# Kernel tuning notes

Hardware: AMD Instinct MI355X
Metric: run time of the kernel (lower is better)

Reference implementation:

```python
import jax, jax.numpy as jnp
import numpy as np

VOCAB, EMBED, HIDDEN = 29, 64, 256
B, SEQ = 8, 257  # T = SEQ-1 = 256


def setup_inputs() -> dict:
    key = jax.random.key(0)
    ks = jax.random.split(key, 16)
    s = 0.02
    embed = jax.random.normal(ks[0], (VOCAB, EMBED), jnp.float32) * s
    embed = embed.at[0].set(0.0)  # padding_idx = PAD_TOKEN = 0
    d = dict(
        x=jax.random.randint(ks[1], (B, SEQ), 0, VOCAB),
        embed=embed,
        W_ih0=jax.random.normal(ks[2], (HIDDEN, EMBED), jnp.float32) * s,
        b_ih0=jax.random.normal(ks[3], (HIDDEN,), jnp.float32) * s,
        W_hh0=jax.random.normal(ks[4], (HIDDEN, HIDDEN), jnp.float32) * s,
        b_hh0=jax.random.normal(ks[5], (HIDDEN,), jnp.float32) * s,
        W_ih1=jax.random.normal(ks[6], (HIDDEN, HIDDEN), jnp.float32) * s,
        b_ih1=jax.random.normal(ks[7], (HIDDEN,), jnp.float32) * s,
        W_hh1=jax.random.normal(ks[8], (HIDDEN, HIDDEN), jnp.float32) * s,
        b_hh1=jax.random.normal(ks[9], (HIDDEN,), jnp.float32) * s,
        Wq=jax.random.normal(ks[10], (HIDDEN, HIDDEN), jnp.float32) * s,
        Wk=jax.random.normal(ks[11], (HIDDEN, HIDDEN), jnp.float32) * s,
        v=jax.random.normal(ks[12], (HIDDEN,), jnp.float32) * s,
        Wfc=jax.random.normal(ks[13], (VOCAB, 2 * HIDDEN), jnp.float32) * s,
        bfc=jax.random.normal(ks[14], (VOCAB,), jnp.float32) * s,
    )
    return d


def _forward(x, embed, W_ih0, b_ih0, W_hh0, b_hh0, W_ih1, b_ih1, W_hh1, b_hh1,
             Wq, Wk, v, Wfc, bfc):
    inp = x[:, :-1]                       # (B, T)
    emb = embed[inp]                      # (B, T, E); dropout = identity (eval)
    Bb, T, _ = emb.shape
    H = W_hh0.shape[0]

    # 2-layer Elman RNN via scan over time
    def step(carry, e_t):
        h0, h1 = carry
        h0 = jnp.tanh(e_t @ W_ih0.T + b_ih0 + h0 @ W_hh0.T + b_hh0)
        h1 = jnp.tanh(h0 @ W_ih1.T + b_ih1 + h1 @ W_hh1.T + b_hh1)
        return (h0, h1), h1

    init = (jnp.zeros((Bb, H), emb.dtype), jnp.zeros((Bb, H), emb.dtype))
    _, hs = jax.lax.scan(step, init, jnp.swapaxes(emb, 0, 1))  # (T, B, H)
    Hs = jnp.swapaxes(hs, 0, 1)           # (B, T, H) = all_hidden

    # Bahdanau additive self-attention over strictly-past hidden states
    q = Hs @ Wq.T                         # (B, T, H)
    k = Hs @ Wk.T                         # (B, T, H)
    e = jnp.tanh(q[:, :, None, :] + k[:, None, :, :])   # (B, T, T, H)
    scores = jnp.einsum('btsh,h->bts', e, v)             # (B, T, T)
    causal = jnp.tril(jnp.ones((T, T), bool), k=-1)      # s < t strictly
    scores = jnp.where(causal[None], scores, jnp.float32(-1e9))
    alpha = jax.nn.softmax(scores, axis=-1)
    ctx = jnp.einsum('bts,bsh->bth', alpha, Hs)          # (B, T, H)
    ctx = ctx * (jnp.arange(T) > 0)[None, :, None]       # t=0: zero context

    out = jnp.concatenate([Hs, ctx], axis=-1) @ Wfc.T + bfc  # (B, T, V)
    return out


def reference(x, embed, W_ih0, b_ih0, W_hh0, b_hh0, W_ih1, b_ih1, W_hh1, b_hh1,
              Wq, Wk, v, Wfc, bfc):
    return _forward(x, embed, W_ih0, b_ih0, W_hh0, b_hh0, W_ih1, b_ih1,
                    W_hh1, b_hh1, Wq, Wk, v, Wfc, bfc)
```

## Files before the change

kernel.cpp:

```cpp
#include <hip/hip_runtime.h>

#define HID   256
#define BATCH 8
#define TT    256
#define SEQL  257
#define VOCAB 29
#define EMB   64
#define TG    4
#define CH    8
#define NCHK  (TT / CH)

typedef _Float16 f16;
typedef f16  f16x8 __attribute__((ext_vector_type(8)));
typedef float f32x4 __attribute__((ext_vector_type(4)));

__device__ __forceinline__ float fast_tanh(float x) {
    float e = exp2f(x * 2.8853900817779268f);
    return 1.0f - 2.0f * __builtin_amdgcn_rcpf(1.0f + e);
}

__global__ __launch_bounds__(256) void pre0_kernel(
    const int* __restrict__ x, const float* __restrict__ embed,
    const float* __restrict__ Wih0, const float* __restrict__ bih0,
    const float* __restrict__ bhh0, float* __restrict__ C0, int* __restrict__ flags)
{
    if (blockIdx.x == 0 && threadIdx.x < 32) flags[threadIdx.x] = 0;
    int b  = blockIdx.x & 7;
    int t0 = (blockIdx.x >> 3) * 8;
    int tid = threadIdx.x;
    __shared__ float er[8][EMB];
    for (int idx = tid; idx < 8 * EMB; idx += 256) {
        int tt = idx >> 6, j = idx & 63;
        er[tt][j] = embed[x[b * SEQL + t0 + tt] * EMB + j];
    }
    __syncthreads();
    int i = tid;
    float base = bih0[i] + bhh0[i];
    float acc[8];
#pragma unroll
    for (int tt = 0; tt < 8; ++tt) acc[tt] = base;
    const float* wr = Wih0 + i * EMB;
    for (int j = 0; j < EMB; j += 4) {
        float4 w = *(const float4*)&wr[j];
#pragma unroll
        for (int tt = 0; tt < 8; ++tt) {
            float4 h = *(const float4*)&er[tt][j];
            acc[tt] += h.x * w.x + h.y * w.y + h.z * w.z + h.w * w.w;
        }
    }
#pragma unroll
    for (int tt = 0; tt < 8; ++tt)
        C0[((t0 + tt) * BATCH + b) * HID + i] = acc[tt];
}

__global__ __launch_bounds__(512) void mega_kernel(
    const float* __restrict__ Whh0, const float* __restrict__ Wih1,
    const float* __restrict__ Whh1, const float* __restrict__ bih1,
    const float* __restrict__ bhh1, const float* __restrict__ Wq,
    const float* __restrict__ Wk, const float* __restrict__ C0,
    float* __restrict__ Q, float* __restrict__ Hs,
    float* __restrict__ tkT, int* __restrict__ flags)
{
    __shared__ f16 hbuf[2][HID];
    __shared__ __align__(16) f16 stg[CH][HID];
    int tid = threadIdx.x;
    int wave = tid >> 6, lane = tid & 63;
    int lrow = lane & 15, lkg = lane >> 4;
    int role = blockIdx.x >> 3;
    int b = blockIdx.x & 7;
    int i0 = wave * 32 + lrow, i1 = i0 + 16;
    const f32x4 Z = {0.f, 0.f, 0.f, 0.f};

#define WAITF(idx, val)                                                             \
    {                                                                               \
        if (tid == 0) {                                                             \
            while (__hip_atomic_load(&flags[idx], __ATOMIC_ACQUIRE,                 \
                                     __HIP_MEMORY_SCOPE_AGENT) < (val))             \
                __builtin_amdgcn_s_sleep(2);                                        \
        }                                                                           \
        __syncthreads();                                                            \
    }
#define POSTF(idx, val)                                                             \
    {                                                                               \
        __syncthreads();                                                            \
        if (tid == 0) {                                                             \
            __hip_atomic_store(&flags[idx], (val), __ATOMIC_RELEASE,                \
                               __HIP_MEMORY_SCOPE_AGENT);                           \
        }                                                                           \
    }

    f16x8 a[8];
#pragma unroll
    for (int kt = 0; kt < 8; ++kt)
#pragma unroll
        for (int e = 0; e < 8; ++e) a[kt][e] = (f16)0.f;

    if (role == 0) {
        for (int idx = tid; idx < 2 * HID; idx += 512) ((f16*)hbuf)[idx] = (f16)0.f;
        f16x8 bf[8][2];
#pragma unroll
        for (int kt = 0; kt < 8; ++kt)
#pragma unroll
            for (int ct = 0; ct < 2; ++ct) {
                int n = wave * 32 + ct * 16 + lrow;
                const float* src = Whh0 + n * HID + kt * 32 + lkg * 8;
                f16x8 v;
#pragma unroll
                for (int e = 0; e < 8; ++e) v[e] = (f16)src[e];
                bf[kt][ct] = v;
            }
        __syncthreads();
        const float* cp = C0 + b * HID;
        float c0 = cp[i0], c1 = cp[i1];
        cp += BATCH * HID;
        f16* hp = (f16*)(Q + (size_t)b * TT * HID);

#define ASTEP(CUR, NXT)                                                             \
    {                                                                               \
        float cn0 = cp[i0];                                                         \
        float cn1 = cp[i1];                                                         \
        cp += BATCH * HID;                                                          \
        if (lrow == 0) {                                                            \
            _Pragma("unroll")                                                       \
            for (int kt = 0; kt < 8; ++kt)                                          \
                a[kt] = *(const f16x8*)&hbuf[CUR][kt * 32 + lkg * 8];               \
        }                                                                           \
        f32x4 p00 = __builtin_amdgcn_mfma_f32_16x16x32_f16(a[0], bf[0][0], Z, 0, 0, 0); \
        f32x4 p01 = __builtin_amdgcn_mfma_f32_16x16x32_f16(a[0], bf[0][1], Z, 0, 0, 0); \
        f32x4 p10 = __builtin_amdgcn_mfma_f32_16x16x32_f16(a[2], bf[2][0], Z, 0, 0, 0); \
        f32x4 p11 = __builtin_amdgcn_mfma_f32_16x16x32_f16(a[2], bf[2][1], Z, 0, 0, 0); \
        f32x4 p20 = __builtin_amdgcn_mfma_f32_16x16x32_f16(a[4], bf[4][0], Z, 0, 0, 0); \
        f32x4 p21 = __builtin_amdgcn_mfma_f32_16x16x32_f16(a[4], bf[4][1], Z, 0, 0, 0); \
        f32x4 p30 = __builtin_amdgcn_mfma_f32_16x16x32_f16(a[6], bf[6][0], Z, 0, 0, 0); \
        f32x4 p31 = __builtin_amdgcn_mfma_f32_16x16x32_f16(a[6], bf[6][1], Z, 0, 0, 0); \
        p00 = __builtin_amdgcn_mfma_f32_16x16x32_f16(a[1], bf[1][0], p00, 0, 0, 0); \
        p01 = __builtin_amdgcn_mfma_f32_16x16x32_f16(a[1], bf[1][1], p01, 0, 0, 0); \
        p10 = __builtin_amdgcn_mfma_f32_16x16x32_f16(a[3], bf[3][0], p10, 0, 0, 0); \
        p11 = __builtin_amdgcn_mfma_f32_16x16x32_f16(a[3], bf[3][1], p11, 0, 0, 0); \
        p20 = __builtin_amdgcn_mfma_f32_16x16x32_f16(a[5], bf[5][0], p20, 0, 0, 0); \
        p21 = __builtin_amdgcn_mfma_f32_16x16x32_f16(a[5], bf[5][1], p21, 0, 0, 0); \
        p30 = __builtin_amdgcn_mfma_f32_16x16x32_f16(a[7], bf[7][0], p30, 0, 0, 0); \
        p31 = __builtin_amdgcn_mfma_f32_16x16x32_f16(a[7], bf[7][1], p31, 0, 0, 0); \
        float v0 = fast_tanh(((p00[0] + p10[0]) + (p20[0] + p30[0])) + c0);         \
        float v1 = fast_tanh(((p01[0] + p11[0]) + (p21[0] + p31[0])) + c1);         \
        f16 hv0 = (f16)v0, hv1 = (f16)v1;                                           \
        if (lane < 16) {                                                            \
            hbuf[NXT][i0] = hv0;                                                    \
            hbuf[NXT][i1] = hv1;                                                    \
            hp[i0] = hv0;                                                           \
            hp[i1] = hv1;                                                           \
        }                                                                           \
        hp += 2 * HID;    \
        c0 = cn0; c1 = cn1;                                                         \
        asm volatile("s_waitcnt lgkmcnt(0)\n\ts_barrier" ::: "memory");             \
    }

        for (int ch = 0; ch < NCHK; ++ch) {
            ASTEP(0, 1) ASTEP(1, 0) ASTEP(0, 1) ASTEP(1, 0)
            ASTEP(0, 1) ASTEP(1, 0) ASTEP(0, 1) ASTEP(1, 0)
            if (ch & 1) POSTF(b, (ch + 1) >> 1)
        }
#undef ASTEP
    } else if (role == 1) {
        f16x8 bfI[8][2];
#pragma unroll
        for (int kt = 0; kt < 8; ++kt)
#pragma unroll
            for (int ct = 0; ct < 2; ++ct) {
                int n = wave * 32 + ct * 16 + lrow;
                const float* src = Wih1 + n * HID + kt * 32 + lkg * 8;
                f16x8 v;
#pragma unroll
                for (int e = 0; e < 8; ++e) v[e] = (f16)src[e];
                bfI[kt][ct] = v;
            }
        int col0 = wave * 32 + (lane & 15), col1 = col0 + 16;
        float bv0 = bih1[col0] + bhh1[col0];
        float bv1 = bih1[col1] + bhh1[col1];
        float* qb = Q + (size_t)b * TT * HID;

#define BBODY(CH_IDX)                                                               \
    {                                                                               \
        int ch = (CH_IDX);                                                          \
        if (tid < 256) {                                                            \
            int tp = tid >> 5, seg = tid & 31;                                      \
            *(f16x8*)&stg[tp][seg * 8] =                                            \
                *(const f16x8*)((const f16*)(qb + (size_t)(ch * CH + tp) * HID) + seg * 8); \
        }                                                                           \
        __syncthreads();                                                            \
        if (lrow < 8) {                                                             \
            _Pragma("unroll")                                                       \
            for (int kt = 0; kt < 8; ++kt)                                          \
                a[kt] = *(const f16x8*)&stg[lrow][kt * 32 + lkg * 8];               \
        }                                                                           \
        f32x4 u0 = __builtin_amdgcn_mfma_f32_16x16x32_f16(a[0], bfI[0][0], Z, 0, 0, 0); \
        f32x4 u1 = __builtin_amdgcn_mfma_f32_16x16x32_f16(a[0], bfI[0][1], Z, 0, 0, 0); \
        _Pragma("unroll")                                                           \
        for (int kt = 1; kt < 8; ++kt) {                                            \
            u0 = __builtin_amdgcn_mfma_f32_16x16x32_f16(a[kt], bfI[kt][0], u0, 0, 0, 0); \
            u1 = __builtin_amdgcn_mfma_f32_16x16x32_f16(a[kt], bfI[kt][1], u1, 0, 0, 0); \
        }                                                                           \
        if (lane < 32) {                                                            \
            float* co = qb + (size_t)(ch * CH + (lane >> 4) * 4) * HID;             \
            co[0 * HID + col0] = u0[0] + bv0;                                       \
            co[1 * HID + col0] = u0[1] + bv0;                                       \
            co[2 * HID + col0] = u0[2] + bv0;                                       \
            co[3 * HID + col0] = u0[3] + bv0;                                       \
            co[0 * HID + col1] = u1[0] + bv1;                                       \
            co[1 * HID + col1] = u1[1] + bv1;                                       \
            co[2 * HID + col1] = u1[2] + bv1;                                       \
            co[3 * HID + col1] = u1[3] + bv1;                                       \
        }                                                                           \
    }

        for (int chp = 0; chp < NCHK / 2; ++chp) {
            WAITF(b, chp + 1)
            BBODY(2 * chp)
            __syncthreads();
            BBODY(2 * chp + 1)
            POSTF(8 + b, chp + 1)
        }
#undef BBODY
    } else if (role == 2) {
        for (int idx = tid; idx < 2 * HID; idx += 512) ((f16*)hbuf)[idx] = (f16)0.f;
        f16x8 bf[8][2];
#pragma unroll
        for (int kt = 0; kt < 8; ++kt)
#pragma unroll
            for (int ct = 0; ct < 2; ++ct) {
                int n = wave * 32 + ct * 16 + lrow;
                const float* src = Whh1 + n * HID + kt * 32 + lkg * 8;
                f16x8 v;
#pragma unroll
                for (int e = 0; e < 8; ++e) v[e] = (f16)src[e];
                bf[kt][ct] = v;
            }
        __syncthreads();
        float* ho = Hs + (size_t)b * TT * HID;
        const float* cq = Q + (size_t)b * TT * HID;

#define CSTEP(CUR, NXT, CV0, CV1)                                                   \
    {                                                                               \
        if (lrow == 0) {                                                            \
            _Pragma("unroll")                                                       \
            for (int kt = 0; kt < 8; ++kt)                                          \
                a[kt] = *(const f16x8*)&hbuf[CUR][kt * 32 + lkg * 8];               \
        }                                                                           \
        f32x4 p00 = __builtin_amdgcn_mfma_f32_16x16x32_f16(a[0], bf[0][0], Z, 0, 0, 0); \
        f32x4 p01 = __builtin_amdgcn_mfma_f32_16x16x32_f16(a[0], bf[0][1], Z, 0, 0, 0); \
        f32x4 p10 = __builtin_amdgcn_mfma_f32_16x16x32_f16(a[2], bf[2][0], Z, 0, 0, 0); \
        f32x4 p11 = __builtin_amdgcn_mfma_f32_16x16x32_f16(a[2], bf[2][1], Z, 0, 0, 0); \
        f32x4 p20 = __builtin_amdgcn_mfma_f32_16x16x32_f16(a[4], bf[4][0], Z, 0, 0, 0); \
        f32x4 p21 = __builtin_amdgcn_mfma_f32_16x16x32_f16(a[4], bf[4][1], Z, 0, 0, 0); \
        f32x4 p30 = __builtin_amdgcn_mfma_f32_16x16x32_f16(a[6], bf[6][0], Z, 0, 0, 0); \
        f32x4 p31 = __builtin_amdgcn_mfma_f32_16x16x32_f16(a[6], bf[6][1], Z, 0, 0, 0); \
        p00 = __builtin_amdgcn_mfma_f32_16x16x32_f16(a[1], bf[1][0], p00, 0, 0, 0); \
        p01 = __builtin_amdgcn_mfma_f32_16x16x32_f16(a[1], bf[1][1], p01, 0, 0, 0); \
        p10 = __builtin_amdgcn_mfma_f32_16x16x32_f16(a[3], bf[3][0], p10, 0, 0, 0); \
        p11 = __builtin_amdgcn_mfma_f32_16x16x32_f16(a[3], bf[3][1], p11, 0, 0, 0); \
        p20 = __builtin_amdgcn_mfma_f32_16x16x32_f16(a[5], bf[5][0], p20, 0, 0, 0); \
        p21 = __builtin_amdgcn_mfma_f32_16x16x32_f16(a[5], bf[5][1], p21, 0, 0, 0); \
        p30 = __builtin_amdgcn_mfma_f32_16x16x32_f16(a[7], bf[7][0], p30, 0, 0, 0); \
        p31 = __builtin_amdgcn_mfma_f32_16x16x32_f16(a[7], bf[7][1], p31, 0, 0, 0); \
        float v0 = fast_tanh(((p00[0] + p10[0]) + (p20[0] + p30[0])) + CV0);        \
        float v1 = fast_tanh(((p01[0] + p11[0]) + (p21[0] + p31[0])) + CV1);        \
        if (lane < 16) {                                                            \
            hbuf[NXT][i0] = (f16)v0;                                                \
            hbuf[NXT][i1] = (f16)v1;                                                \
            ho[i0] = v0;                                                            \
            ho[i1] = v1;                                                            \
        }                                                                           \
        ho += HID;                                                                  \
        asm volatile("s_waitcnt lgkmcnt(0)\n\ts_barrier" ::: "memory");             \
    }

#define CCHUNK(CH_IDX)                                                              \
    {                                                                               \
        const float* cc = cq + (size_t)(CH_IDX) * CH * HID;                         \
        float d00 = cc[0*HID+i0], d01 = cc[0*HID+i1];                               \
        float d10 = cc[1*HID+i0], d11 = cc[1*HID+i1];                               \
        float d20 = cc[2*HID+i0], d21 = cc[2*HID+i1];                               \
        float d30 = cc[3*HID+i0], d31 = cc[3*HID+i1];                               \
        float d40 = cc[4*HID+i0], d41 = cc[4*HID+i1];                               \
        float d50 = cc[5*HID+i0], d51 = cc[5*HID+i1];                               \
        float d60 = cc[6*HID+i0], d61 = cc[6*HID+i1];                               \
        float d70 = cc[7*HID+i0], d71 = cc[7*HID+i1];                               \
        CSTEP(0, 1, d00, d01) CSTEP(1, 0, d10, d11)                                 \
        CSTEP(0, 1, d20, d21) CSTEP(1, 0, d30, d31)                                 \
        CSTEP(0, 1, d40, d41) CSTEP(1, 0, d50, d51)                                 \
        CSTEP(0, 1, d60, d61) CSTEP(1, 0, d70, d71)                                 \
    }

        for (int chp = 0; chp < NCHK / 2; ++chp) {
            WAITF(8 + b, chp + 1)
            CCHUNK(2 * chp)
            CCHUNK(2 * chp + 1)
            POSTF(16 + b, chp + 1)
        }
#undef CCHUNK
#undef CSTEP
    } else {
        const float* W = (role == 3) ? Wq : Wk;
        f16x8 bfW[8][2];
#pragma unroll
        for (int kt = 0; kt < 8; ++kt)
#pragma unroll
            for (int ct = 0; ct < 2; ++ct) {
                int n = wave * 32 + ct * 16 + lrow;
                const float* src = W + n * HID + kt * 32 + lkg * 8;
                f16x8 v;
#pragma unroll
                for (int e = 0; e < 8; ++e) v[e] = (f16)src[e];
                bfW[kt][ct] = v;
            }
        int col0 = wave * 32 + (lane & 15), col1 = col0 + 16;
        const float* hsb = Hs + (size_t)b * TT * HID;
        float* qb = Q + (size_t)b * TT * HID;

#define DEBODY(CH_IDX)                                                              \
    {                                                                               \
        int ch = (CH_IDX);                                                          \
        if (tid < 256) {                                                            \
            const float* src = hsb + (size_t)ch * CH * HID + tid * 8;               \
            float4 v0 = *(const float4*)&src[0];                                    \
            float4 v1 = *(const float4*)&src[4];                                    \
            f16x8 h = { (f16)v0.x, (f16)v0.y, (f16)v0.z, (f16)v0.w,                 \
                        (f16)v1.x, (f16)v1.y, (f16)v1.z, (f16)v1.w };               \
            *(f16x8*)((f16*)stg + tid * 8) = h;                                     \
        }                                                                           \
        __syncthreads();                                                            \
        if (lrow < 8) {                                                             \
            _Pragma("unroll")                                                       \
            for (int kt = 0; kt < 8; ++kt)                                          \
                a[kt] = *(const f16x8*)&stg[lrow][kt * 32 + lkg * 8];               \
        }                                                                           \
        f32x4 u0 = __builtin_amdgcn_mfma_f32_16x16x32_f16(a[0], bfW[0][0], Z, 0, 0, 0); \
        f32x4 u1 = __builtin_amdgcn_mfma_f32_16x16x32_f16(a[0], bfW[0][1], Z, 0, 0, 0); \
        _Pragma("unroll")                                                           \
        for (int kt = 1; kt < 8; ++kt) {                                            \
            u0 = __builtin_amdgcn_mfma_f32_16x16x32_f16(a[kt], bfW[kt][0], u0, 0, 0, 0); \
            u1 = __builtin_amdgcn_mfma_f32_16x16x32_f16(a[kt], bfW[kt][1], u1, 0, 0, 0); \
        }                                                                           \
        if (lane < 32) {                                                            \
            int tb2 = ch * CH + (lane >> 4) * 4;                                    \
            if (role == 3) {                                                        \
                float* co = qb + (size_t)tb2 * HID;                                 \
                co[0 * HID + col0] = fast_tanh(u0[0]);                              \
                co[1 * HID + col0] = fast_tanh(u0[1]);                              \
                co[2 * HID + col0] = fast_tanh(u0[2]);                              \
                co[3 * HID + col0] = fast_tanh(u0[3]);                              \
                co[0 * HID + col1] = fast_tanh(u1[0]);                              \
                co[1 * HID + col1] = fast_tanh(u1[1]);                              \
                co[2 * HID + col1] = fast_tanh(u1[2]);                              \
                co[3 * HID + col1] = fast_tanh(u1[3]);                              \
            } else {                                                                \
                float4 s0 = { fast_tanh(u0[0]), fast_tanh(u0[1]),                   \
                              fast_tanh(u0[2]), fast_tanh(u0[3]) };                 \
                float4 s1 = { fast_tanh(u1[0]), fast_tanh(u1[1]),                   \
                              fast_tanh(u1[2]), fast_tanh(u1[3]) };                 \
                *(float4*)&tkT[((size_t)b * HID + col0) * TT + tb2] = s0;           \
                *(float4*)&tkT[((size_t)b * HID + col1) * TT + tb2] = s1;           \
            }                                                                       \
        }                                                                           \
        __syncthreads();                                                            \
    }

        for (int chp = 0; chp < NCHK / 2; ++chp) {
            WAITF(16 + b, chp + 1)
            DEBODY(2 * chp + 0)
            DEBODY(2 * chp + 1)
        }
#undef DEBODY
    }
#undef WAITF
#undef POSTF
}

__global__ __launch_bounds__(256) void attn_kernel(
    const float* __restrict__ tq, const float* __restrict__ tkT,
    const float* __restrict__ vvec, const float* __restrict__ Hs,
    const float* __restrict__ Wfc, const float* __restrict__ bfc,
    float* __restrict__ out)
{
    int b  = blockIdx.x & 7;
    int t0 = (blockIdx.x >> 3) * TG;
    int tid = threadIdx.x;
    int wave = tid >> 6, lane = tid & 63;
    __shared__ float qs[TG][HID], vs[HID], alpha[TG][HID];
    __shared__ float cvec[TG][8][68];
    __shared__ float redm[4][TG], reds[4][TG];
#pragma unroll
    for (int j = 0; j < TG; ++j)
        qs[j][tid] = tq[((size_t)b * TT + t0 + j) * HID + tid];
    vs[tid] = vvec[tid];
    __syncthreads();

    float sc[TG];
#pragma unroll
    for (int j = 0; j < TG; ++j) sc[j] = -1e30f;
    if ((wave << 6) < t0 + TG) {
        const float* kT = tkT + (size_t)b * HID * TT + tid;
        float a0 = 0.f, a1 = 0.f, a2 = 0.f, a3 = 0.f;
        for (int jj = 0; jj < HID; jj += 4) {
            float k0 = kT[(size_t)(jj + 0) * TT];
            float k1 = kT[(size_t)(jj + 1) * TT];
            float k2 = kT[(size_t)(jj + 2) * TT];
            float k3 = kT[(size_t)(jj + 3) * TT];
            float4 vv = *(const float4*)&vs[jj];
            float4 q0 = *(const float4*)&qs[0][jj];
            float4 q1 = *(const float4*)&qs[1][jj];
            float4 q2 = *(const float4*)&qs[2][jj];
            float4 q3 = *(const float4*)&qs[3][jj];
#define TADD(qc, kc, vc, acc) { float num = qc + kc; float den = __builtin_fmaf(qc, kc, 1.f); acc += vc * num * __builtin_amdgcn_rcpf(den); }
            TADD(q0.x, k0, vv.x, a0) TADD(q0.y, k1, vv.y, a0) TADD(q0.z, k2, vv.z, a0) TADD(q0.w, k3, vv.w, a0)
            TADD(q1.x, k0, vv.x, a1) TADD(q1.y, k1, vv.y, a1) TADD(q1.z, k2, vv.z, a1) TADD(q1.w, k3, vv.w, a1)
            TADD(q2.x, k0, vv.x, a2) TADD(q2.y, k1, vv.y, a2) TADD(q2.z, k2, vv.z, a2) TADD(q2.w, k3, vv.w, a2)
            TADD(q3.x, k0, vv.x, a3) TADD(q3.y, k1, vv.y, a3) TADD(q3.z, k2, vv.z, a3) TADD(q3.w, k3, vv.w, a3)
#undef TADD
        }
        if (tid < t0 + 0) sc[0] = a0;
        if (tid < t0 + 1) sc[1] = a1;
        if (tid < t0 + 2) sc[2] = a2;
        if (tid < t0 + 3) sc[3] = a3;
    }
    float m0 = sc[0], m1 = sc[1], m2 = sc[2], m3 = sc[3];
#pragma unroll
    for (int off = 32; off; off >>= 1) {
        m0 = fmaxf(m0, __shfl_down(m0, off));
        m1 = fmaxf(m1, __shfl_down(m1, off));
        m2 = fmaxf(m2, __shfl_down(m2, off));
        m3 = fmaxf(m3, __shfl_down(m3, off));
    }
    if (lane == 0) { redm[wave][0] = m0; redm[wave][1] = m1; redm[wave][2] = m2; redm[wave][3] = m3; }
    __syncthreads();
    float ej[TG];
#pragma unroll
    for (int j = 0; j < TG; ++j) {
        float m = fmaxf(fmaxf(redm[0][j], redm[1][j]), fmaxf(redm[2][j], redm[3][j]));
        ej[j] = (tid < t0 + j) ? exp2f((sc[j] - m) * 1.4426950408889634f) : 0.f;
    }
    float z0 = ej[0], z1 = ej[1], z2 = ej[2], z3 = ej[3];
#pragma unroll
    for (int off = 32; off; off >>= 1) {
        z0 += __shfl_down(z0, off);
        z1 += __shfl_down(z1, off);
        z2 += __shfl_down(z2, off);
        z3 += __shfl_down(z3, off);
    }
    if (lane == 0) { reds[wave][0] = z0; reds[wave][1] = z1; reds[wave][2] = z2; reds[wave][3] = z3; }
    __syncthreads();
#pragma unroll
    for (int j = 0; j < TG; ++j) {
        float z = reds[0][j] + reds[1][j] + reds[2][j] + reds[3][j];
        alpha[j][tid] = (t0 + j == 0) ? 0.f : ej[j] * __builtin_amdgcn_rcpf(z);
    }
    __syncthreads();

    float c0 = 0.f, c1 = 0.f, c2 = 0.f, c3 = 0.f;
    const float* hb = Hs + (size_t)b * TT * HID;
    for (int s = 0; s < t0 + TG; s += 4) {
        float4 av0 = *(const float4*)&alpha[0][s];
        float4 av1 = *(const float4*)&alpha[1][s];
        float4 av2 = *(const float4*)&alpha[2][s];
        float4 av3 = *(const float4*)&alpha[3][s];
        float h0 = hb[(s + 0) * HID + tid];
        float h1 = hb[(s + 1) * HID + tid];
        float h2 = hb[(s + 2) * HID + tid];
        float h3 = hb[(s + 3) * HID + tid];
        c0 += av0.x * h0 + av0.y * h1 + av0.z * h2 + av0.w * h3;
        c1 += av1.x * h0 + av1.y * h1 + av1.z * h2 + av1.w * h3;
        c2 += av2.x * h0 + av2.y * h1 + av2.z * h2 + av2.w * h3;
        c3 += av3.x * h0 + av3.y * h1 + av3.z * h2 + av3.w * h3;
    }
    {
        int ph = tid >> 6, jj = tid & 63;
        cvec[0][ph][jj] = hb[(size_t)(t0 + 0) * HID + tid]; cvec[0][4 + ph][jj] = c0;
        cvec[1][ph][jj] = hb[(size_t)(t0 + 1) * HID + tid]; cvec[1][4 + ph][jj] = c1;
        cvec[2][ph][jj] = hb[(size_t)(t0 + 2) * HID + tid]; cvec[2][4 + ph][jj] = c2;
        cvec[3][ph][jj] = hb[(size_t)(t0 + 3) * HID + tid]; cvec[3][4 + ph][jj] = c3;
    }
    __syncthreads();

    if (tid < VOCAB * 8) {
        int o = tid >> 3, p = tid & 7;
        const float* wr = Wfc + o * 2 * HID + p * 64;
#pragma unroll
        for (int j = 0; j < TG; ++j) {
            const float* cv = &cvec[j][p][0];
            float a = 0.f;
            for (int jj = 0; jj < 64; jj += 4) {
                float4 w  = *(const float4*)&wr[jj];
                float4 cc = *(const float4*)&cv[jj];
                a += w.x * cc.x + w.y * cc.y + w.z * cc.z + w.w * cc.w;
            }
            a += __shfl_down(a, 4);
            a += __shfl_down(a, 2);
            a += __shfl_down(a, 1);
            if (p == 0) out[((size_t)b * TT + t0 + j) * VOCAB + o] = a + bfc[o];
        }
    }
}

extern "C" void kernel_launch(void* const* d_in, const int* in_sizes, int n_in,
                              void* d_out, int out_size, void* d_ws, size_t ws_size,
                              hipStream_t stream)
{
    (void)in_sizes; (void)n_in; (void)out_size; (void)ws_size;
    const int*   x     = (const int*)d_in[0];
    const float* embed = (const float*)d_in[1];
    const float* Wih0  = (const float*)d_in[2];
    const float* bih0  = (const float*)d_in[3];
    const float* Whh0  = (const float*)d_in[4];
    const float* bhh0  = (const float*)d_in[5];
    const float* Wih1  = (const float*)d_in[6];
    const float* bih1  = (const float*)d_in[7];
    const float* Whh1  = (const float*)d_in[8];
    const float* bhh1  = (const float*)d_in[9];
    const float* Wq    = (const float*)d_in[10];
    const float* Wk    = (const float*)d_in[11];
    const float* vvec  = (const float*)d_in[12];
    const float* Wfc   = (const float*)d_in[13];
    const float* bfc   = (const float*)d_in[14];
    float* out = (float*)d_out;
    float* ws  = (float*)d_ws;

    const size_t SZ = (size_t)TT * BATCH * HID;
    float* C0  = ws;
    float* Hs  = ws + SZ;
    float* Q   = ws + 2 * SZ;
    float* tkT = ws + 3 * SZ;
    int* flags = (int*)d_out;

    pre0_kernel<<<256, 256, 0, stream>>>(x, embed, Wih0, bih0, bhh0, C0, flags);
    mega_kernel<<<40, 512, 0, stream>>>(Whh0, Wih1, Whh1, bih1, bhh1, Wq, Wk,
                                        C0, Q, Hs, tkT, flags);
    attn_kernel<<<512, 256, 0, stream>>>(Q, tkT, vvec, Hs, Wfc, bfc, out);
}
```

Baseline: 209.7 us.

## Fuse attention into the persistent RNN kernel with flag-gated consumer blocks

Removes the separate attention kernel and appends its work as extra blocks of the mega kernel. Each attention block spin-waits on new per-batch Q/K progress flags that the projection roles now post. This lets attention for early timesteps overlap the remaining recurrence and removes a kernel launch boundary. Flags move from the output buffer to a device global, and shared memory becomes a union; the risks are that spinning blocks compete for CU resources with the producer blocks and that half of each 512-thread attention block sits idle.

```diff
diff --git a/kernel.cpp b/kernel.cpp
--- a/kernel.cpp
+++ b/kernel.cpp
@@ -14,6 +14,8 @@
 typedef f16  f16x8 __attribute__((ext_vector_type(8)));
 typedef float f32x4 __attribute__((ext_vector_type(4)));
 
+__device__ int g_flags[48];
+
 __device__ __forceinline__ float fast_tanh(float x) {
     float e = exp2f(x * 2.8853900817779268f);
     return 1.0f - 2.0f * __builtin_amdgcn_rcpf(1.0f + e);
@@ -22,9 +24,9 @@
 __global__ __launch_bounds__(256) void pre0_kernel(
     const int* __restrict__ x, const float* __restrict__ embed,
     const float* __restrict__ Wih0, const float* __restrict__ bih0,
-    const float* __restrict__ bhh0, float* __restrict__ C0, int* __restrict__ flags)
+    const float* __restrict__ bhh0, float* __restrict__ C0)
 {
-    if (blockIdx.x == 0 && threadIdx.x < 32) flags[threadIdx.x] = 0;
+    if (blockIdx.x == 0 && threadIdx.x < 48) g_flags[threadIdx.x] = 0;
     int b  = blockIdx.x & 7;
     int t0 = (blockIdx.x >> 3) * 8;
     int tid = threadIdx.x;
@@ -53,20 +55,25 @@
         C0[((t0 + tt) * BATCH + b) * HID + i] = acc[tt];
 }
 
+struct SmemM { f16 hbuf[2][HID]; __align__(16) f16 stg[CH][HID]; };
+struct SmemA { float qs[TG][HID]; float vs[HID]; float alpha[TG][HID];
+               float cvec[TG][8][68]; float redm[4][TG]; float reds[4][TG]; };
+union SmemU { SmemM m; SmemA a; };
+
 __global__ __launch_bounds__(512) void mega_kernel(
     const float* __restrict__ Whh0, const float* __restrict__ Wih1,
     const float* __restrict__ Whh1, const float* __restrict__ bih1,
     const float* __restrict__ bhh1, const float* __restrict__ Wq,
     const float* __restrict__ Wk, const float* __restrict__ C0,
-    float* __restrict__ Q, float* __restrict__ Hs,
-    float* __restrict__ tkT, int* __restrict__ flags)
+    float* __restrict__ Q, float* __restrict__ Hs, float* __restrict__ tkT,
+    const float* __restrict__ vvec, const float* __restrict__ Wfc,
+    const float* __restrict__ bfc, float* __restrict__ out)
 {
-    __shared__ f16 hbuf[2][HID];
-    __shared__ __align__(16) f16 stg[CH][HID];
+    __shared__ SmemU smem;
     int tid = threadIdx.x;
     int wave = tid >> 6, lane = tid & 63;
     int lrow = lane & 15, lkg = lane >> 4;
-    int role = blockIdx.x >> 3;
+    int role = (blockIdx.x < 40) ? (blockIdx.x >> 3) : 5;
     int b = blockIdx.x & 7;
     int i0 = wave * 32 + lrow, i1 = i0 + 16;
     const f32x4 Z = {0.f, 0.f, 0.f, 0.f};
@@ -74,7 +81,7 @@
 #define WAITF(idx, val)                                                             \
     {                                                                               \
         if (tid == 0) {                                                             \
-            while (__hip_atomic_load(&flags[idx], __ATOMIC_ACQUIRE,                 \
+            while (__hip_atomic_load(&g_flags[idx], __ATOMIC_ACQUIRE,               \
                                      __HIP_MEMORY_SCOPE_AGENT) < (val))             \
                 __builtin_amdgcn_s_sleep(2);                                        \
         }                                                                           \
@@ -84,7 +91,7 @@
     {                                                                               \
         __syncthreads();                                                            \
         if (tid == 0) {                                                             \
-            __hip_atomic_store(&flags[idx], (val), __ATOMIC_RELEASE,                \
+            __hip_atomic_store(&g_flags[idx], (val), __ATOMIC_RELEASE,              \
                                __HIP_MEMORY_SCOPE_AGENT);                           \
         }                                                                           \
     }
@@ -96,6 +103,7 @@
         for (int e = 0; e < 8; ++e) a[kt][e] = (f16)0.f;
 
     if (role == 0) {
+        f16 (*hbuf)[HID] = smem.m.hbuf;
         for (int idx = tid; idx < 2 * HID; idx += 512) ((f16*)hbuf)[idx] = (f16)0.f;
         f16x8 bf[8][2];
 #pragma unroll
@@ -162,6 +170,7 @@
         }
 #undef ASTEP
     } else if (role == 1) {
+        f16 (*stg)[HID] = smem.m.stg;
         f16x8 bfI[8][2];
 #pragma unroll
         for (int kt = 0; kt < 8; ++kt)
@@ -222,6 +231,7 @@
         }
 #undef BBODY
     } else if (role == 2) {
+        f16 (*hbuf)[HID] = smem.m.hbuf;
         for (int idx = tid; idx < 2 * HID; idx += 512) ((f16*)hbuf)[idx] = (f16)0.f;
         f16x8 bf[8][2];
 #pragma unroll
@@ -299,7 +309,8 @@
         }
 #undef CCHUNK
 #undef CSTEP
-    } else {
+    } else if (role <= 4) {
+        f16 (*stg)[HID] = smem.m.stg;
         const float* W = (role == 3) ? Wq : Wk;
         f16x8 bfW[8][2];
 #pragma unroll
@@ -369,136 +380,146 @@
             WAITF(16 + b, chp + 1)
             DEBODY(2 * chp + 0)
             DEBODY(2 * chp + 1)
+            POSTF(24 + (role - 3) * 8 + b, chp + 1)
         }
 #undef DEBODY
+    } else {
+        int aidx = blockIdx.x - 40;
+        int ab = aidx & 7;
+        int t0 = (aidx >> 3) * TG;
+        int p_need = (t0 + TG + 15) / 16;
+        WAITF(24 + ab, p_need)
+        WAITF(32 + ab, p_need)
+
+        float (*qs)[HID]     = smem.a.qs;
+        float* vs            = smem.a.vs;
+        float (*alpha)[HID]  = smem.a.alpha;
+        float (*cvec)[8][68] = smem.a.cvec;
+        float (*redm)[TG]    = smem.a.redm;
+        float (*reds)[TG]    = smem.a.reds;
+        const float* tq = Q;
+
+        if (tid < HID) {
+#pragma unroll
+            for (int j = 0; j < TG; ++j)
+                qs[j][tid] = tq[((size_t)ab * TT + t0 + j) * HID + tid];
+            vs[tid] = vvec[tid];
+        }
+        __syncthreads();
+
+        float sc[TG];
+#pragma unroll
+        for (int j = 0; j < TG; ++j) sc[j] = -1e30f;
+        if ((wave << 6) < t0 + TG) {
+            const float* kT = tkT + (size_t)ab * HID * TT + tid;
+            float a0 = 0.f, a1 = 0.f, a2 = 0.f, a3 = 0.f;
+            for (int jj = 0; jj < HID; jj += 4) {
+                float k0 = kT[(size_t)(jj + 0) * TT];
+                float k1 = kT[(size_t)(jj + 1) * TT];
+                float k2 = kT[(size_t)(jj + 2) * TT];
+                float k3 = kT[(size_t)(jj + 3) * TT];
+                float4 vv = *(const float4*)&vs[jj];
+                float4 q0 = *(const float4*)&qs[0][jj];
+                float4 q1 = *(const float4*)&qs[1][jj];
+                float4 q2 = *(const float4*)&qs[2][jj];
+                float4 q3 = *(const float4*)&qs[3][jj];
+#define TADD(qc, kc, vc, acc) { float num = qc + kc; float den = __builtin_fmaf(qc, kc, 1.f); acc += vc * num * __builtin_amdgcn_rcpf(den); }
+                TADD(q0.x, k0, vv.x, a0) TADD(q0.y, k1, vv.y, a0) TADD(q0.z, k2, vv.z, a0) TADD(q0.w, k3, vv.w, a0)
+                TADD(q1.x, k0, vv.x, a1) TADD(q1.y, k1, vv.y, a1) TADD(q1.z, k2, vv.z, a1) TADD(q1.w, k3, vv.w, a1)
+                TADD(q2.x, k0, vv.x, a2) TADD(q2.y, k1, vv.y, a2) TADD(q2.z, k2, vv.z, a2) TADD(q2.w, k3, vv.w, a2)
+                TADD(q3.x, k0, vv.x, a3) TADD(q3.y, k1, vv.y, a3) TADD(q3.z, k2, vv.z, a3) TADD(q3.w, k3, vv.w, a3)
+#undef TADD
+            }
+            if (tid < t0 + 0) sc[0] = a0;
+            if (tid < t0 + 1) sc[1] = a1;
+            if (tid < t0 + 2) sc[2] = a2;
+            if (tid < t0 + 3) sc[3] = a3;
+        }
+        float m0 = sc[0], m1 = sc[1], m2 = sc[2], m3 = sc[3];
+#pragma unroll
+        for (int off = 32; off; off >>= 1) {
+            m0 = fmaxf(m0, __shfl_down(m0, off));
+            m1 = fmaxf(m1, __shfl_down(m1, off));
+            m2 = fmaxf(m2, __shfl_down(m2, off));
+            m3 = fmaxf(m3, __shfl_down(m3, off));
+        }
+        if (lane == 0 && wave < 4) {
+            redm[wave][0] = m0; redm[wave][1] = m1; redm[wave][2] = m2; redm[wave][3] = m3;
+        }
+        __syncthreads();
+        float ej[TG];
+#pragma unroll
+        for (int j = 0; j < TG; ++j) {
+            float m = fmaxf(fmaxf(redm[0][j], redm[1][j]), fmaxf(redm[2][j], redm[3][j]));
+            ej[j] = (tid < t0 + j) ? exp2f((sc[j] - m) * 1.4426950408889634f) : 0.f;
+        }
+        float z0 = ej[0], z1 = ej[1], z2 = ej[2], z3 = ej[3];
+#pragma unroll
+        for (int off = 32; off; off >>= 1) {
+            z0 += __shfl_down(z0, off);
+            z1 += __shfl_down(z1, off);
+            z2 += __shfl_down(z2, off);
+            z3 += __shfl_down(z3, off);
+        }
+        if (lane == 0 && wave < 4) {
+            reds[wave][0] = z0; reds[wave][1] = z1; reds[wave][2] = z2; reds[wave][3] = z3;
+        }
+        __syncthreads();
+        if (tid < HID) {
+#pragma unroll
+            for (int j = 0; j < TG; ++j) {
+                float z = reds[0][j] + reds[1][j] + reds[2][j] + reds[3][j];
+                alpha[j][tid] = (t0 + j == 0) ? 0.f : ej[j] * __builtin_amdgcn_rcpf(z);
+            }
+        }
+        __syncthreads();
+
+        if (tid < HID) {
+            float c0 = 0.f, c1 = 0.f, c2 = 0.f, c3 = 0.f;
+            const float* hb = Hs + (size_t)ab * TT * HID;
+            for (int s = 0; s < t0 + TG; s += 4) {
+                float4 av0 = *(const float4*)&alpha[0][s];
+                float4 av1 = *(const float4*)&alpha[1][s];
+                float4 av2 = *(const float4*)&alpha[2][s];
+                float4 av3 = *(const float4*)&alpha[3][s];
+                float h0 = hb[(s + 0) * HID + tid];
+                float h1 = hb[(s + 1) * HID + tid];
+                float h2 = hb[(s + 2) * HID + tid];
+                float h3 = hb[(s + 3) * HID + tid];
+                c0 += av0.x * h0 + av0.y * h1 + av0.z * h2 + av0.w * h3;
+                c1 += av1.x * h0 + av1.y * h1 + av1.z * h2 + av1.w * h3;
+                c2 += av2.x * h0 + av2.y * h1 + av2.z * h2 + av2.w * h3;
+                c3 += av3.x * h0 + av3.y * h1 + av3.z * h2 + av3.w * h3;
+            }
+            int ph = tid >> 6, jj = tid & 63;
+            cvec[0][ph][jj] = hb[(size_t)(t0 + 0) * HID + tid]; cvec[0][4 + ph][jj] = c0;
+            cvec[1][ph][jj] = hb[(size_t)(t0 + 1) * HID + tid]; cvec[1][4 + ph][jj] = c1;
+            cvec[2][ph][jj] = hb[(size_t)(t0 + 2) * HID + tid]; cvec[2][4 + ph][jj] = c2;
+            cvec[3][ph][jj] = hb[(size_t)(t0 + 3) * HID + tid]; cvec[3][4 + ph][jj] = c3;
+        }
+        __syncthreads();
+
+        if (tid < VOCAB * 8) {
+            int o = tid >> 3, p = tid & 7;
+            const float* wr = Wfc + o * 2 * HID + p * 64;
+#pragma unroll
+            for (int j = 0; j < TG; ++j) {
+                const float* cv = &cvec[j][p][0];
+                float acc = 0.f;
+                for (int jj = 0; jj < 64; jj += 4) {
+                    float4 w  = *(const float4*)&wr[jj];
+                    float4 cc = *(const float4*)&cv[jj];
+                    acc += w.x * cc.x + w.y * cc.y + w.z * cc.z + w.w * cc.w;
+                }
+                acc += __shfl_down(acc, 4);
+                acc += __shfl_down(acc, 2);
+                acc += __shfl_down(acc, 1);
+                if (p == 0) out[((size_t)ab * TT + t0 + j) * VOCAB + o] = acc + bfc[o];
+            }
+        }
     }
 #undef WAITF
 #undef POSTF
-}
-
-__global__ __launch_bounds__(256) void attn_kernel(
-    const float* __restrict__ tq, const float* __restrict__ tkT,
-    const float* __restrict__ vvec, const float* __restrict__ Hs,
-    const float* __restrict__ Wfc, const float* __restrict__ bfc,
-    float* __restrict__ out)
-{
-    int b  = blockIdx.x & 7;
-    int t0 = (blockIdx.x >> 3) * TG;
-    int tid = threadIdx.x;
-    int wave = tid >> 6, lane = tid & 63;
-    __shared__ float qs[TG][HID], vs[HID], alpha[TG][HID];
-    __shared__ float cvec[TG][8][68];
-    __shared__ float redm[4][TG], reds[4][TG];
-#pragma unroll
-    for (int j = 0; j < TG; ++j)
-        qs[j][tid] = tq[((size_t)b * TT + t0 + j) * HID + tid];
-    vs[tid] = vvec[tid];
-    __syncthreads();
-
-    float sc[TG];
-#pragma unroll
-    for (int j = 0; j < TG; ++j) sc[j] = -1e30f;
-    if ((wave << 6) < t0 + TG) {
-        const float* kT = tkT + (size_t)b * HID * TT + tid;
-        float a0 = 0.f, a1 = 0.f, a2 = 0.f, a3 = 0.f;
-        for (int jj = 0; jj < HID; jj += 4) {
-            float k0 = kT[(size_t)(jj + 0) * TT];
-            float k1 = kT[(size_t)(jj + 1) * TT];
-            float k2 = kT[(size_t)(jj + 2) * TT];
-            float k3 = kT[(size_t)(jj + 3) * TT];
-            float4 vv = *(const float4*)&vs[jj];
-            float4 q0 = *(const float4*)&qs[0][jj];
-            float4 q1 = *(const float4*)&qs[1][jj];
-            float4 q2 = *(const float4*)&qs[2][jj];
-            float4 q3 = *(const float4*)&qs[3][jj];
-#define TADD(qc, kc, vc, acc) { float num = qc + kc; float den = __builtin_fmaf(qc, kc, 1.f); acc += vc * num * __builtin_amdgcn_rcpf(den); }
-            TADD(q0.x, k0, vv.x, a0) TADD(q0.y, k1, vv.y, a0) TADD(q0.z, k2, vv.z, a0) TADD(q0.w, k3, vv.w, a0)
-            TADD(q1.x, k0, vv.x, a1) TADD(q1.y, k1, vv.y, a1) TADD(q1.z, k2, vv.z, a1) TADD(q1.w, k3, vv.w, a1)
-            TADD(q2.x, k0, vv.x, a2) TADD(q2.y, k1, vv.y, a2) TADD(q2.z, k2, vv.z, a2) TADD(q2.w, k3, vv.w, a2)
-            TADD(q3.x, k0, vv.x, a3) TADD(q3.y, k1, vv.y, a3) TADD(q3.z, k2, vv.z, a3) TADD(q3.w, k3, vv.w, a3)
-#undef TADD
-        }
-        if (tid < t0 + 0) sc[0] = a0;
-        if (tid < t0 + 1) sc[1] = a1;
-        if (tid < t0 + 2) sc[2] = a2;
-        if (tid < t0 + 3) sc[3] = a3;
-    }
-    float m0 = sc[0], m1 = sc[1], m2 = sc[2], m3 = sc[3];
-#pragma unroll
-    for (int off = 32; off; off >>= 1) {
-        m0 = fmaxf(m0, __shfl_down(m0, off));
-        m1 = fmaxf(m1, __shfl_down(m1, off));
-        m2 = fmaxf(m2, __shfl_down(m2, off));
-        m3 = fmaxf(m3, __shfl_down(m3, off));
-    }
-    if (lane == 0) { redm[wave][0] = m0; redm[wave][1] = m1; redm[wave][2] = m2; redm[wave][3] = m3; }
-    __syncthreads();
-    float ej[TG];
-#pragma unroll
-    for (int j = 0; j < TG; ++j) {
-        float m = fmaxf(fmaxf(redm[0][j], redm[1][j]), fmaxf(redm[2][j], redm[3][j]));
-        ej[j] = (tid < t0 + j) ? exp2f((sc[j] - m) * 1.4426950408889634f) : 0.f;
-    }
-    float z0 = ej[0], z1 = ej[1], z2 = ej[2], z3 = ej[3];
-#pragma unroll
-    for (int off = 32; off; off >>= 1) {
-        z0 += __shfl_down(z0, off);
-        z1 += __shfl_down(z1, off);
-        z2 += __shfl_down(z2, off);
-        z3 += __shfl_down(z3, off);
-    }
-    if (lane == 0) { reds[wave][0] = z0; reds[wave][1] = z1; reds[wave][2] = z2; reds[wave][3] = z3; }
-    __syncthreads();
-#pragma unroll
-    for (int j = 0; j < TG; ++j) {
-        float z = reds[0][j] + reds[1][j] + reds[2][j] + reds[3][j];
-        alpha[j][tid] = (t0 + j == 0) ? 0.f : ej[j] * __builtin_amdgcn_rcpf(z);
-    }
-    __syncthreads();
-
-    float c0 = 0.f, c1 = 0.f, c2 = 0.f, c3 = 0.f;
-    const float* hb = Hs + (size_t)b * TT * HID;
-    for (int s = 0; s < t0 + TG; s += 4) {
-        float4 av0 = *(const float4*)&alpha[0][s];
-        float4 av1 = *(const float4*)&alpha[1][s];
-        float4 av2 = *(const float4*)&alpha[2][s];
-        float4 av3 = *(const float4*)&alpha[3][s];
-        float h0 = hb[(s + 0) * HID + tid];
-        float h1 = hb[(s + 1) * HID + tid];
-        float h2 = hb[(s + 2) * HID + tid];
-        float h3 = hb[(s + 3) * HID + tid];
-        c0 += av0.x * h0 + av0.y * h1 + av0.z * h2 + av0.w * h3;
-        c1 += av1.x * h0 + av1.y * h1 + av1.z * h2 + av1.w * h3;
-        c2 += av2.x * h0 + av2.y * h1 + av2.z * h2 + av2.w * h3;
-        c3 += av3.x * h0 + av3.y * h1 + av3.z * h2 + av3.w * h3;
-    }
-    {
-        int ph = tid >> 6, jj = tid & 63;
-        cvec[0][ph][jj] = hb[(size_t)(t0 + 0) * HID + tid]; cvec[0][4 + ph][jj] = c0;
-        cvec[1][ph][jj] = hb[(size_t)(t0 + 1) * HID + tid]; cvec[1][4 + ph][jj] = c1;
-        cvec[2][ph][jj] = hb[(size_t)(t0 + 2) * HID + tid]; cvec[2][4 + ph][jj] = c2;
-        cvec[3][ph][jj] = hb[(size_t)(t0 + 3) * HID + tid]; cvec[3][4 + ph][jj] = c3;
-    }
-    __syncthreads();
-
-    if (tid < VOCAB * 8) {
-        int o = tid >> 3, p = tid & 7;
-        const float* wr = Wfc + o * 2 * HID + p * 64;
-#pragma unroll
-        for (int j = 0; j < TG; ++j) {
-            const float* cv = &cvec[j][p][0];
-            float a = 0.f;
-            for (int jj = 0; jj < 64; jj += 4) {
-                float4 w  = *(const float4*)&wr[jj];
-                float4 cc = *(const float4*)&cv[jj];
-                a += w.x * cc.x + w.y * cc.y + w.z * cc.z + w.w * cc.w;
-            }
-            a += __shfl_down(a, 4);
-            a += __shfl_down(a, 2);
-            a += __shfl_down(a, 1);
-            if (p == 0) out[((size_t)b * TT + t0 + j) * VOCAB + o] = a + bfc[o];
-        }
-    }
 }
 
 extern "C" void kernel_launch(void* const* d_in, const int* in_sizes, int n_in,
@@ -529,10 +550,9 @@
     float* Hs  = ws + SZ;
     float* Q   = ws + 2 * SZ;
     float* tkT = ws + 3 * SZ;
-    int* flags = (int*)d_out;
-
-    pre0_kernel<<<256, 256, 0, stream>>>(x, embed, Wih0, bih0, bhh0, C0, flags);
-    mega_kernel<<<40, 512, 0, stream>>>(Whh0, Wih1, Whh1, bih1, bhh1, Wq, Wk,
-                                        C0, Q, Hs, tkT, flags);
-    attn_kernel<<<512, 256, 0, stream>>>(Q, tkT, vvec, Hs, Wfc, bfc, out);
+
+    pre0_kernel<<<256, 256, 0, stream>>>(x, embed, Wih0, bih0, bhh0, C0);
+    mega_kernel<<<40 + BATCH * (TT / TG), 512, 0, stream>>>(
+        Whh0, Wih1, Whh1, bih1, bhh1, Wq, Wk, C0, Q, Hs, tkT,
+        vvec, Wfc, bfc, out);
 }
```

Result: slower. 295.0 us (+40.6%).
